# Performance work log

Hardware: AMD Instinct MI355X
Metric: run time of the kernel (lower is better)

The kernel has to match this reference:

```python
import jax, jax.numpy as jnp
import numpy as np

N_NODES = 100000
N_EDGES = 1600000
F_IN = 64
F_HID = 64
F_OUT = 64
N_HEADS = 4


def setup_inputs() -> dict:
    key = jax.random.key(0)
    ks = jax.random.split(key, 7)
    h = jax.random.normal(ks[0], (N_NODES, F_IN), dtype=jnp.float32)
    src = jax.random.randint(ks[1], (N_EDGES,), 0, N_NODES, dtype=jnp.int32)
    dst = jax.random.randint(ks[2], (N_EDGES,), 0, N_NODES, dtype=jnp.int32)
    s = 1.0 / np.sqrt(F_IN)
    Wk = jax.random.normal(ks[3], (F_IN, F_HID), dtype=jnp.float32) * s
    Wq = jax.random.normal(ks[4], (F_IN, F_HID), dtype=jnp.float32) * s
    W = jax.random.normal(ks[5], (F_IN, F_OUT), dtype=jnp.float32) * s
    b = jnp.zeros((F_OUT,), dtype=jnp.float32)
    return {"h": h, "src": src, "dst": dst, "Wk": Wk, "Wq": Wq, "W": W, "b": b,
            "num_heads": N_HEADS}


def reference(h, src, dst, Wk, Wq, W, b, num_heads):
    N = h.shape[0]
    H = num_heads
    # k, q: [N, H, Dh]
    k = (h @ Wk).reshape(N, H, -1)
    q = (h @ Wq).reshape(N, H, -1)
    # edge scores e[e,h] = <k[src], q[dst]>  (u_dot_v)
    e = jnp.einsum('ehd,ehd->eh', k[src], q[dst])  # [E, H]
    # edge softmax over incoming edges of each destination node (per head)
    m = jax.ops.segment_max(e, dst, num_segments=N)          # [N, H]
    m = jax.lax.stop_gradient(m)
    ex = jnp.exp(e - m[dst])                                  # [E, H]
    z = jax.ops.segment_sum(ex, dst, num_segments=N)          # [N, H]
    a = ex / z[dst]                                           # [E, H]
    # message m = u_mul_e(h, a): broadcast (F,) with (H,1) -> [E, H, F]; sum to dst
    msg = h[src][:, None, :] * a[:, :, None]                  # [E, H, F]
    hn = jax.ops.segment_sum(msg, dst, num_segments=N)        # [N, H, F]
    out = hn @ W + b                                          # [N, H, F_out]
    return out.reshape(N, -1)                                 # [N, H*F_out]
```

## Files before the change

### kernel.cpp

```cpp
#include <hip/hip_runtime.h>
#include <hip/hip_fp16.h>
#include <math.h>


#define FDIM 64
#define NHEADS 4
#define TILE 8192
#define BCAP 6144

typedef float f32x2 __attribute__((ext_vector_type(2)));

__global__ __launch_bounds__(256) void k1_kernel(
    const float* __restrict__ h, const float* __restrict__ Wk,
    const float* __restrict__ Wq, const float* __restrict__ Wo,
    const int* __restrict__ src, const int* __restrict__ dst,
    __half* __restrict__ k16, __half* __restrict__ q16,
    __half* __restrict__ hp16, int* __restrict__ gcnt,
    unsigned int* __restrict__ ebuf,
    int N, int E, int KQB, int PB, int nbuck)
{
    __shared__ __align__(16) unsigned char smem_raw[39936];
    int bid = blockIdx.x;
    int t = threadIdx.x;
    if (bid < KQB) {
        float* sWk = (float*)smem_raw;
        float* sWq = (float*)(smem_raw + 16384);
        for (int i = t; i < FDIM * FDIM; i += 256) {
            sWk[i] = Wk[i] * 1.4426950408889634f;
            sWq[i] = Wq[i];
        }
        __syncthreads();
        int cg = t & 3;
        int rg = t >> 2;
        long base = (long)bid * 128 + rg * 2;
        const float4* sWk4 = (const float4*)sWk;
        const float4* sWq4 = (const float4*)sWq;
        const float4* h4 = (const float4*)h;
        float acck[2][16], accq[2][16];
#pragma unroll
        for (int i = 0; i < 2; ++i)
#pragma unroll
            for (int c = 0; c < 16; ++c) { acck[i][c] = 0.f; accq[i][c] = 0.f; }

        for (int fs = 0; fs < FDIM; fs += 4) {
            float4 hv[2];
#pragma unroll
            for (int i = 0; i < 2; ++i) {
                long r = base + i; if (r >= N) r = N - 1;
                hv[i] = h4[r * 16 + (fs >> 2)];
            }
#pragma unroll
            for (int fi = 0; fi < 4; ++fi) {
                int f = fs + fi;
                float4 wk0 = sWk4[f * 16 + cg * 4 + 0];
                float4 wk1 = sWk4[f * 16 + cg * 4 + 1];
                float4 wk2 = sWk4[f * 16 + cg * 4 + 2];
                float4 wk3 = sWk4[f * 16 + cg * 4 + 3];
                float4 wq0 = sWq4[f * 16 + cg * 4 + 0];
                float4 wq1 = sWq4[f * 16 + cg * 4 + 1];
                float4 wq2 = sWq4[f * 16 + cg * 4 + 2];
                float4 wq3 = sWq4[f * 16 + cg * 4 + 3];
#pragma unroll
                for (int i = 0; i < 2; ++i) {
                    float hvf = (&hv[i].x)[fi];
                    acck[i][0]  = fmaf(hvf, wk0.x, acck[i][0]);
                    acck[i][1]  = fmaf(hvf, wk0.y, acck[i][1]);
                    acck[i][2]  = fmaf(hvf, wk0.z, acck[i][2]);
                    acck[i][3]  = fmaf(hvf, wk0.w, acck[i][3]);
                    acck[i][4]  = fmaf(hvf, wk1.x, acck[i][4]);
                    acck[i][5]  = fmaf(hvf, wk1.y, acck[i][5]);
                    acck[i][6]  = fmaf(hvf, wk1.z, acck[i][6]);
                    acck[i][7]  = fmaf(hvf, wk1.w, acck[i][7]);
                    acck[i][8]  = fmaf(hvf, wk2.x, acck[i][8]);
                    acck[i][9]  = fmaf(hvf, wk2.y, acck[i][9]);
                    acck[i][10] = fmaf(hvf, wk2.z, acck[i][10]);
                    acck[i][11] = fmaf(hvf, wk2.w, acck[i][11]);
                    acck[i][12] = fmaf(hvf, wk3.x, acck[i][12]);
                    acck[i][13] = fmaf(hvf, wk3.y, acck[i][13]);
                    acck[i][14] = fmaf(hvf, wk3.z, acck[i][14]);
                    acck[i][15] = fmaf(hvf, wk3.w, acck[i][15]);
                    accq[i][0]  = fmaf(hvf, wq0.x, accq[i][0]);
                    accq[i][1]  = fmaf(hvf, wq0.y, accq[i][1]);
                    accq[i][2]  = fmaf(hvf, wq0.z, accq[i][2]);
                    accq[i][3]  = fmaf(hvf, wq0.w, accq[i][3]);
                    accq[i][4]  = fmaf(hvf, wq1.x, accq[i][4]);
                    accq[i][5]  = fmaf(hvf, wq1.y, accq[i][5]);
                    accq[i][6]  = fmaf(hvf, wq1.z, accq[i][6]);
                    accq[i][7]  = fmaf(hvf, wq1.w, accq[i][7]);
                    accq[i][8]  = fmaf(hvf, wq2.x, accq[i][8]);
                    accq[i][9]  = fmaf(hvf, wq2.y, accq[i][9]);
                    accq[i][10] = fmaf(hvf, wq2.z, accq[i][10]);
                    accq[i][11] = fmaf(hvf, wq2.w, accq[i][11]);
                    accq[i][12] = fmaf(hvf, wq3.x, accq[i][12]);
                    accq[i][13] = fmaf(hvf, wq3.y, accq[i][13]);
                    accq[i][14] = fmaf(hvf, wq3.z, accq[i][14]);
                    accq[i][15] = fmaf(hvf, wq3.w, accq[i][15]);
                }
            }
        }
#pragma unroll
        for (int i = 0; i < 2; ++i) {
            long r = base + i;
            if (r >= N) continue;
            __half2 hk[8], hq[8];
#pragma unroll
            for (int c = 0; c < 8; ++c) {
                hk[c] = __floats2half2_rn(acck[i][2 * c], acck[i][2 * c + 1]);
                hq[c] = __floats2half2_rn(accq[i][2 * c], accq[i][2 * c + 1]);
            }
            float4* kout = (float4*)(k16 + (size_t)r * FDIM + cg * 16);
            float4* qout = (float4*)(q16 + (size_t)r * FDIM + cg * 16);
            kout[0] = ((float4*)hk)[0]; kout[1] = ((float4*)hk)[1];
            qout[0] = ((float4*)hq)[0]; qout[1] = ((float4*)hq)[1];
        }
    } else if (bid < KQB + PB) {
        float* sW = (float*)smem_raw;
        for (int i = t; i < FDIM * FDIM; i += 256) sW[i] = Wo[i];
        __syncthreads();
        int cg = t & 3;
        int rg = t >> 2;
        long base = (long)(bid - KQB) * 128 + rg * 2;
        const float4* sW4 = (const float4*)sW;
        const float4* h4 = (const float4*)h;
        float accp[2][16];
#pragma unroll
        for (int i = 0; i < 2; ++i)
#pragma unroll
            for (int c = 0; c < 16; ++c) accp[i][c] = 0.f;

        for (int fs = 0; fs < FDIM; fs += 4) {
            float4 hv[2];
#pragma unroll
            for (int i = 0; i < 2; ++i) {
                long r = base + i; if (r >= N) r = N - 1;
                hv[i] = h4[r * 16 + (fs >> 2)];
            }
#pragma unroll
            for (int fi = 0; fi < 4; ++fi) {
                int f = fs + fi;
                float4 w0 = sW4[f * 16 + cg * 4 + 0];
                float4 w1 = sW4[f * 16 + cg * 4 + 1];
                float4 w2 = sW4[f * 16 + cg * 4 + 2];
                float4 w3 = sW4[f * 16 + cg * 4 + 3];
#pragma unroll
                for (int i = 0; i < 2; ++i) {
                    float hvf = (&hv[i].x)[fi];
                    accp[i][0]  = fmaf(hvf, w0.x, accp[i][0]);
                    accp[i][1]  = fmaf(hvf, w0.y, accp[i][1]);
                    accp[i][2]  = fmaf(hvf, w0.z, accp[i][2]);
                    accp[i][3]  = fmaf(hvf, w0.w, accp[i][3]);
                    accp[i][4]  = fmaf(hvf, w1.x, accp[i][4]);
                    accp[i][5]  = fmaf(hvf, w1.y, accp[i][5]);
                    accp[i][6]  = fmaf(hvf, w1.z, accp[i][6]);
                    accp[i][7]  = fmaf(hvf, w1.w, accp[i][7]);
                    accp[i][8]  = fmaf(hvf, w2.x, accp[i][8]);
                    accp[i][9]  = fmaf(hvf, w2.y, accp[i][9]);
                    accp[i][10] = fmaf(hvf, w2.z, accp[i][10]);
                    accp[i][11] = fmaf(hvf, w2.w, accp[i][11]);
                    accp[i][12] = fmaf(hvf, w3.x, accp[i][12]);
                    accp[i][13] = fmaf(hvf, w3.y, accp[i][13]);
                    accp[i][14] = fmaf(hvf, w3.z, accp[i][14]);
                    accp[i][15] = fmaf(hvf, w3.w, accp[i][15]);
                }
            }
        }
#pragma unroll
        for (int i = 0; i < 2; ++i) {
            long r = base + i;
            if (r >= N) continue;
            __half2 hp[8];
#pragma unroll
            for (int c = 0; c < 8; ++c)
                hp[c] = __floats2half2_rn(accp[i][2 * c], accp[i][2 * c + 1]);
            float4* pout = (float4*)(hp16 + (size_t)r * FDIM + cg * 16);
            pout[0] = ((float4*)hp)[0];
            pout[1] = ((float4*)hp)[1];
        }
    } else {
        unsigned int* bh     = (unsigned int*)smem_raw;
        unsigned int* bstart = bh + 512;
        unsigned int* bbase  = bstart + 512;
        unsigned int* sd     = bbase + 512;
        unsigned int* ebuf_l = sd + 256;
        long e0 = (long)(bid - KQB - PB) * TILE;
        int cnt_tile = (int)(((long)E - e0 < (long)TILE) ? ((long)E - e0) : (long)TILE);

        bh[t] = 0; bh[t + 256] = 0;
        __syncthreads();
        for (int j = t; j < cnt_tile; j += 256)
            atomicAdd(&bh[dst[e0 + j] >> 8], 1u);
        __syncthreads();
        unsigned int c0 = bh[2 * t], c1 = bh[2 * t + 1];
        unsigned int s = c0 + c1;
        sd[t] = s;
        __syncthreads();
        for (int off = 1; off < 256; off <<= 1) {
            unsigned int v = (t >= off) ? sd[t - off] : 0;
            __syncthreads();
            sd[t] += v;
            __syncthreads();
        }
        unsigned int ex = sd[t] - s;
        bh[2 * t] = ex;          bstart[2 * t] = ex;
        bh[2 * t + 1] = ex + c0; bstart[2 * t + 1] = ex + c0;
        if (c0 > 0) bbase[2 * t] = (unsigned int)atomicAdd(&gcnt[2 * t], (int)c0);
        if (c1 > 0) bbase[2 * t + 1] = (unsigned int)atomicAdd(&gcnt[2 * t + 1], (int)c1);
        __syncthreads();
        for (int j = t; j < cnt_tile; j += 256) {
            int d = dst[e0 + j];
            int sv = src[e0 + j];
            unsigned int pos = atomicAdd(&bh[d >> 8], 1u);
            ebuf_l[pos] = ((unsigned int)sv << 8) | (unsigned int)(d & 255);
        }
        __syncthreads();
        int wave = t >> 6, lane = t & 63;
        for (int b = wave; b < nbuck; b += 4) {
            unsigned int st = bstart[b];
            unsigned int en = bh[b];
            if (st == en) continue;
            unsigned int gb = bbase[b];
            if (gb >= (unsigned int)BCAP) continue;
            unsigned int room = (unsigned int)BCAP - gb;
            if (en - st > room) en = st + room;
            unsigned int* dstp = ebuf + (size_t)b * BCAP + gb;
            for (unsigned int j = st + lane; j < en; j += 64)
                dstp[j - st] = ebuf_l[j];
        }
    }
}

__global__ __launch_bounds__(256) void binB_kernel(
    const int* __restrict__ gcnt, const unsigned int* __restrict__ ebuf,
    int* __restrict__ rowptr, int* __restrict__ srcs, int N)
{
    __shared__ int sg[512];
    __shared__ unsigned int lh[256];
    __shared__ unsigned int sd[256];
    __shared__ unsigned int srcs_l[BCAP];
    int t = threadIdx.x;
    int b = blockIdx.x;

    int c0 = gcnt[2 * t], c1 = gcnt[2 * t + 1];
    int ssum = c0 + c1;
    sd[t] = (unsigned int)ssum;
    __syncthreads();
    for (int off = 1; off < 256; off <<= 1) {
        unsigned int v = (t >= off) ? sd[t - off] : 0;
        __syncthreads();
        sd[t] += v;
        __syncthreads();
    }
    int ex = (int)sd[t] - ssum;
    sg[2 * t] = ex;
    sg[2 * t + 1] = ex + c0;
    __syncthreads();
    int gb = sg[b];
    int cnt = gcnt[b];
    if (cnt > BCAP) cnt = BCAP;
    int n0 = b << 8;
    const unsigned int* eb = ebuf + (size_t)b * BCAP;

    lh[t] = 0;
    __syncthreads();
    for (int j = t; j < cnt; j += 256)
        atomicAdd(&lh[eb[j] & 255u], 1u);
    __syncthreads();
    unsigned int c = lh[t];
    sd[t] = c;
    __syncthreads();
    for (int off = 1; off < 256; off <<= 1) {
        unsigned int v = (t >= off) ? sd[t - off] : 0;
        __syncthreads();
        sd[t] += v;
        __syncthreads();
    }
    unsigned int excl = sd[t] - c;
    lh[t] = excl;
    if (n0 + t < N) rowptr[n0 + t] = gb + (int)excl;
    __syncthreads();
    for (int j = t; j < cnt; j += 256) {
        unsigned int p = eb[j];
        unsigned int pos = atomicAdd(&lh[p & 255u], 1u);
        srcs_l[pos] = p >> 8;
    }
    __syncthreads();
    for (int j = t; j < cnt; j += 256)
        srcs[gb + j] = (int)srcs_l[j];
}

__device__ __forceinline__ float dot16(const float4* kk, const float* qf) {
    const __half2* kh = (const __half2*)kk;
    float acc = 0.f;
#pragma unroll
    for (int j = 0; j < 8; ++j) {
        float2 kf = __half22float2(kh[j]);
        acc = fmaf(kf.x, qf[2 * j], acc);
        acc = fmaf(kf.y, qf[2 * j + 1], acc);
    }
    return acc;
}

__device__ __forceinline__ void agg2f(
    float w0, float w1, float w2, float w3, __half2 g,
    f32x2& a0, f32x2& a1, f32x2& a2, f32x2& a3)
{
    float2 f2 = __half22float2(g);
    f32x2 hv; hv.x = f2.x; hv.y = f2.y;
    f32x2 wv;
    wv.x = w0; wv.y = w0; a0 = __builtin_elementwise_fma(wv, hv, a0);
    wv.x = w1; wv.y = w1; a1 = __builtin_elementwise_fma(wv, hv, a1);
    wv.x = w2; wv.y = w2; a2 = __builtin_elementwise_fma(wv, hv, a2);
    wv.x = w3; wv.y = w3; a3 = __builtin_elementwise_fma(wv, hv, a3);
}

__global__ __launch_bounds__(256) void fused_sa_kernel(
    const int* __restrict__ rowptr, const int* __restrict__ srcs,
    const __half* __restrict__ k16, const __half* __restrict__ q16,
    const __half* __restrict__ hp16, const float* __restrict__ bvec,
    float* __restrict__ out, int N, int E)
{
    int lane = threadIdx.x & 63;
    int n = blockIdx.x * 4 + (threadIdx.x >> 6);
    if (n >= N) return;
    int start = rowptr[n];
    int end   = (n == N - 1) ? E : rowptr[n + 1];

    int hh   = lane & 3;
    int rr   = lane >> 2;
    int half = lane >> 5;
    int fl   = lane & 31;

    const float4* qp = (const float4*)(q16 + (size_t)n * FDIM + hh * 16);
    float4 qv[2] = { qp[0], qp[1] };
    const __half2* qh = (const __half2*)qv;
    float qf[16];
#pragma unroll
    for (int j = 0; j < 8; ++j) {
        float2 f = __half22float2(qh[j]);
        qf[2 * j] = f.x;
        qf[2 * j + 1] = f.y;
    }

    float zacc = 0.f;
    f32x2 a0 = {0.f, 0.f}, a1 = {0.f, 0.f}, a2 = {0.f, 0.f}, a3 = {0.f, 0.f};

    for (int base = start; base < end; base += 16) {
        int idx = base + rr;
        bool valid = (idx < end);
        int ic = valid ? idx : (end - 1);
        int sA = srcs[ic];
        const float4* kp = (const float4*)(k16 + (size_t)sA * FDIM + hh * 16);
        float4 ka[2] = { kp[0], kp[1] };
        float w = __builtin_amdgcn_exp2f(dot16(ka, qf));
        w = valid ? w : 0.f;
        zacc += w;

#pragma unroll
        for (int j = 0; j < 2; ++j) {
            int g0i = base + j * 8;
            if (g0i < end) {
                int rb = j * 8 + half;
                int s0 = __shfl(sA, (rb + 0) * 4, 64);
                int s1 = __shfl(sA, (rb + 2) * 4, 64);
                int s2 = __shfl(sA, (rb + 4) * 4, 64);
                int s3 = __shfl(sA, (rb + 6) * 4, 64);
                __half2 g0 = *((const __half2*)(hp16 + (size_t)s0 * FDIM) + fl);
                __half2 g1 = *((const __half2*)(hp16 + (size_t)s1 * FDIM) + fl);
                __half2 g2 = *((const __half2*)(hp16 + (size_t)s2 * FDIM) + fl);
                __half2 g3 = *((const __half2*)(hp16 + (size_t)s3 * FDIM) + fl);
                float wa0 = __shfl(w, (rb + 0) * 4 + 0, 64);
                float wa1 = __shfl(w, (rb + 0) * 4 + 1, 64);
                float wa2 = __shfl(w, (rb + 0) * 4 + 2, 64);
                float wa3 = __shfl(w, (rb + 0) * 4 + 3, 64);
                agg2f(wa0, wa1, wa2, wa3, g0, a0, a1, a2, a3);
                float wb0 = __shfl(w, (rb + 2) * 4 + 0, 64);
                float wb1 = __shfl(w, (rb + 2) * 4 + 1, 64);
                float wb2 = __shfl(w, (rb + 2) * 4 + 2, 64);
                float wb3 = __shfl(w, (rb + 2) * 4 + 3, 64);
                agg2f(wb0, wb1, wb2, wb3, g1, a0, a1, a2, a3);
                float wc0 = __shfl(w, (rb + 4) * 4 + 0, 64);
                float wc1 = __shfl(w, (rb + 4) * 4 + 1, 64);
                float wc2 = __shfl(w, (rb + 4) * 4 + 2, 64);
                float wc3 = __shfl(w, (rb + 4) * 4 + 3, 64);
                agg2f(wc0, wc1, wc2, wc3, g2, a0, a1, a2, a3);
                float wd0 = __shfl(w, (rb + 6) * 4 + 0, 64);
                float wd1 = __shfl(w, (rb + 6) * 4 + 1, 64);
                float wd2 = __shfl(w, (rb + 6) * 4 + 2, 64);
                float wd3 = __shfl(w, (rb + 6) * 4 + 3, 64);
                agg2f(wd0, wd1, wd2, wd3, g3, a0, a1, a2, a3);
            }
        }
    }

    zacc += __shfl_xor(zacc, 4, 64);
    zacc += __shfl_xor(zacc, 8, 64);
    zacc += __shfl_xor(zacc, 16, 64);
    zacc += __shfl_xor(zacc, 32, 64);
    float z0 = __shfl(zacc, 0, 64);
    float z1 = __shfl(zacc, 1, 64);
    float z2 = __shfl(zacc, 2, 64);
    float z3 = __shfl(zacc, 3, 64);

    a0.x += __shfl_xor(a0.x, 32, 64); a0.y += __shfl_xor(a0.y, 32, 64);
    a1.x += __shfl_xor(a1.x, 32, 64); a1.y += __shfl_xor(a1.y, 32, 64);
    a2.x += __shfl_xor(a2.x, 32, 64); a2.y += __shfl_xor(a2.y, 32, 64);
    a3.x += __shfl_xor(a3.x, 32, 64); a3.y += __shfl_xor(a3.y, 32, 64);

    if (half != 0) return;
    float bv0 = bvec[2 * fl], bv1 = bvec[2 * fl + 1];
    float2* o = (float2*)(out + (size_t)n * (NHEADS * FDIM));
    if (end > start) {
        float rz0 = 1.f / z0;
        float rz1 = 1.f / z1;
        float rz2 = 1.f / z2;
        float rz3 = 1.f / z3;
        o[fl]      = make_float2(fmaf(a0.x, rz0, bv0), fmaf(a0.y, rz0, bv1));
        o[32 + fl] = make_float2(fmaf(a1.x, rz1, bv0), fmaf(a1.y, rz1, bv1));
        o[64 + fl] = make_float2(fmaf(a2.x, rz2, bv0), fmaf(a2.y, rz2, bv1));
        o[96 + fl] = make_float2(fmaf(a3.x, rz3, bv0), fmaf(a3.y, rz3, bv1));
    } else {
        float2 bz = make_float2(bv0, bv1);
        o[fl] = bz; o[32 + fl] = bz; o[64 + fl] = bz; o[96 + fl] = bz;
    }
}

extern "C" void kernel_launch(void* const* d_in, const int* in_sizes, int n_in,
                              void* d_out, int out_size, void* d_ws, size_t ws_size,
                              hipStream_t stream) {
    const float* h   = (const float*)d_in[0];
    const int*   src = (const int*)d_in[1];
    const int*   dst = (const int*)d_in[2];
    const float* Wk  = (const float*)d_in[3];
    const float* Wq  = (const float*)d_in[4];
    const float* W   = (const float*)d_in[5];
    const float* b   = (const float*)d_in[6];
    float* out = (float*)d_out;

    const int N = in_sizes[0] / FDIM;
    const int E = in_sizes[1];

    const int NBUCK = (N + 255) >> 8;
    const int NTILE = (E + TILE - 1) / TILE;
    const int KQB   = (N + 127) / 128;
    const int PB    = (N + 127) / 128;

    __half* k16 = (__half*)d_ws;
    __half* q16 = k16 + (size_t)N * FDIM;
    __half* hp16 = q16 + (size_t)N * FDIM;
    unsigned int* ebuf = (unsigned int*)(hp16 + (size_t)N * FDIM);
    int* srcs   = (int*)(ebuf + (size_t)NBUCK * BCAP);
    int* gcnt   = srcs + E;
    int* rowptr = gcnt + 512;

    hipMemsetAsync(gcnt, 0, 512 * sizeof(int), stream);

    k1_kernel<<<KQB + PB + NTILE, 256, 0, stream>>>(
        h, Wk, Wq, W, src, dst, k16, q16, hp16, gcnt, ebuf,
        N, E, KQB, PB, NBUCK);
    binB_kernel<<<NBUCK, 256, 0, stream>>>(gcnt, ebuf, rowptr, srcs, N);
    fused_sa_kernel<<<(N + 3) / 4, 256, 0, stream>>>(
        rowptr, srcs, k16, q16, hp16, b, out, N, E);
}
```

Baseline: 332.5 us.

## Use 8-byte gathers with four edges per wave step and cache bucket entries in LDS

The aggregation loop in the fused kernel now splits the wave into four quarter-waves, each gathering a 4-half (8-byte) slice of a source row. It processes one edge per quarter per step, giving four iterations of one load instead of two iterations of four 4-byte loads. That means fewer but wider gather instructions and fewer weight shuffles per edge, with twice the accumulators and a two-stage cross-lane reduction at the end. Separately, binB now keeps the bucket's edge list in shared memory after the first read so the scatter pass does not re-read global memory, at the cost of an extra 24KB of LDS per block.

New measurement: 317.4 us. -4.6%, faster.

```diff
diff --git a/kernel.cpp b/kernel.cpp
--- a/kernel.cpp
+++ b/kernel.cpp
@@ -236,6 +236,7 @@
     __shared__ int sg[512];
     __shared__ unsigned int lh[256];
     __shared__ unsigned int sd[256];
+    __shared__ unsigned int ebuf_l[BCAP];
     __shared__ unsigned int srcs_l[BCAP];
     int t = threadIdx.x;
     int b = blockIdx.x;
@@ -243,6 +244,7 @@
     int c0 = gcnt[2 * t], c1 = gcnt[2 * t + 1];
     int ssum = c0 + c1;
     sd[t] = (unsigned int)ssum;
+    lh[t] = 0;
     __syncthreads();
     for (int off = 1; off < 256; off <<= 1) {
         unsigned int v = (t >= off) ? sd[t - off] : 0;
@@ -260,10 +262,11 @@
     int n0 = b << 8;
     const unsigned int* eb = ebuf + (size_t)b * BCAP;
 
-    lh[t] = 0;
-    __syncthreads();
-    for (int j = t; j < cnt; j += 256)
-        atomicAdd(&lh[eb[j] & 255u], 1u);
+    for (int j = t; j < cnt; j += 256) {
+        unsigned int p = eb[j];
+        ebuf_l[j] = p;
+        atomicAdd(&lh[p & 255u], 1u);
+    }
     __syncthreads();
     unsigned int c = lh[t];
     sd[t] = c;
@@ -279,7 +282,7 @@
     if (n0 + t < N) rowptr[n0 + t] = gb + (int)excl;
     __syncthreads();
     for (int j = t; j < cnt; j += 256) {
-        unsigned int p = eb[j];
+        unsigned int p = ebuf_l[j];
         unsigned int pos = atomicAdd(&lh[p & 255u], 1u);
         srcs_l[pos] = p >> 8;
     }
@@ -298,19 +301,6 @@
         acc = fmaf(kf.y, qf[2 * j + 1], acc);
     }
     return acc;
-}
-
-__device__ __forceinline__ void agg2f(
-    float w0, float w1, float w2, float w3, __half2 g,
-    f32x2& a0, f32x2& a1, f32x2& a2, f32x2& a3)
-{
-    float2 f2 = __half22float2(g);
-    f32x2 hv; hv.x = f2.x; hv.y = f2.y;
-    f32x2 wv;
-    wv.x = w0; wv.y = w0; a0 = __builtin_elementwise_fma(wv, hv, a0);
-    wv.x = w1; wv.y = w1; a1 = __builtin_elementwise_fma(wv, hv, a1);
-    wv.x = w2; wv.y = w2; a2 = __builtin_elementwise_fma(wv, hv, a2);
-    wv.x = w3; wv.y = w3; a3 = __builtin_elementwise_fma(wv, hv, a3);
 }
 
 __global__ __launch_bounds__(256) void fused_sa_kernel(
@@ -325,10 +315,10 @@
     int start = rowptr[n];
     int end   = (n == N - 1) ? E : rowptr[n + 1];
 
-    int hh   = lane & 3;
-    int rr   = lane >> 2;
-    int half = lane >> 5;
-    int fl   = lane & 31;
+    int hh = lane & 3;
+    int rr = lane >> 2;
+    int qt = lane >> 4;
+    int fq = lane & 15;
 
     const float4* qp = (const float4*)(q16 + (size_t)n * FDIM + hh * 16);
     float4 qv[2] = { qp[0], qp[1] };
@@ -342,7 +332,10 @@
     }
 
     float zacc = 0.f;
-    f32x2 a0 = {0.f, 0.f}, a1 = {0.f, 0.f}, a2 = {0.f, 0.f}, a3 = {0.f, 0.f};
+    f32x2 a00 = {0.f,0.f}, a01 = {0.f,0.f};
+    f32x2 a10 = {0.f,0.f}, a11 = {0.f,0.f};
+    f32x2 a20 = {0.f,0.f}, a21 = {0.f,0.f};
+    f32x2 a30 = {0.f,0.f}, a31 = {0.f,0.f};
 
     for (int base = start; base < end; base += 16) {
         int idx = base + rr;
@@ -356,38 +349,32 @@
         zacc += w;
 
 #pragma unroll
-        for (int j = 0; j < 2; ++j) {
-            int g0i = base + j * 8;
-            if (g0i < end) {
-                int rb = j * 8 + half;
-                int s0 = __shfl(sA, (rb + 0) * 4, 64);
-                int s1 = __shfl(sA, (rb + 2) * 4, 64);
-                int s2 = __shfl(sA, (rb + 4) * 4, 64);
-                int s3 = __shfl(sA, (rb + 6) * 4, 64);
-                __half2 g0 = *((const __half2*)(hp16 + (size_t)s0 * FDIM) + fl);
-                __half2 g1 = *((const __half2*)(hp16 + (size_t)s1 * FDIM) + fl);
-                __half2 g2 = *((const __half2*)(hp16 + (size_t)s2 * FDIM) + fl);
-                __half2 g3 = *((const __half2*)(hp16 + (size_t)s3 * FDIM) + fl);
-                float wa0 = __shfl(w, (rb + 0) * 4 + 0, 64);
-                float wa1 = __shfl(w, (rb + 0) * 4 + 1, 64);
-                float wa2 = __shfl(w, (rb + 0) * 4 + 2, 64);
-                float wa3 = __shfl(w, (rb + 0) * 4 + 3, 64);
-                agg2f(wa0, wa1, wa2, wa3, g0, a0, a1, a2, a3);
-                float wb0 = __shfl(w, (rb + 2) * 4 + 0, 64);
-                float wb1 = __shfl(w, (rb + 2) * 4 + 1, 64);
-                float wb2 = __shfl(w, (rb + 2) * 4 + 2, 64);
-                float wb3 = __shfl(w, (rb + 2) * 4 + 3, 64);
-                agg2f(wb0, wb1, wb2, wb3, g1, a0, a1, a2, a3);
-                float wc0 = __shfl(w, (rb + 4) * 4 + 0, 64);
-                float wc1 = __shfl(w, (rb + 4) * 4 + 1, 64);
-                float wc2 = __shfl(w, (rb + 4) * 4 + 2, 64);
-                float wc3 = __shfl(w, (rb + 4) * 4 + 3, 64);
-                agg2f(wc0, wc1, wc2, wc3, g2, a0, a1, a2, a3);
-                float wd0 = __shfl(w, (rb + 6) * 4 + 0, 64);
-                float wd1 = __shfl(w, (rb + 6) * 4 + 1, 64);
-                float wd2 = __shfl(w, (rb + 6) * 4 + 2, 64);
-                float wd3 = __shfl(w, (rb + 6) * 4 + 3, 64);
-                agg2f(wd0, wd1, wd2, wd3, g3, a0, a1, a2, a3);
+        for (int k = 0; k < 4; ++k) {
+            if (base + k * 4 < end) {
+                int rloc = k * 4 + qt;
+                int sB = __shfl(sA, rloc * 4, 64);
+                uint2 g = *(const uint2*)(hp16 + (size_t)sB * FDIM + fq * 4);
+                float w0 = __shfl(w, rloc * 4 + 0, 64);
+                float w1 = __shfl(w, rloc * 4 + 1, 64);
+                float w2 = __shfl(w, rloc * 4 + 2, 64);
+                float w3 = __shfl(w, rloc * 4 + 3, 64);
+                float2 flo = __half22float2(*(__half2*)&g.x);
+                float2 fhi = __half22float2(*(__half2*)&g.y);
+                f32x2 vlo; vlo.x = flo.x; vlo.y = flo.y;
+                f32x2 vhi; vhi.x = fhi.x; vhi.y = fhi.y;
+                f32x2 wv;
+                wv.x = w0; wv.y = w0;
+                a00 = __builtin_elementwise_fma(wv, vlo, a00);
+                a01 = __builtin_elementwise_fma(wv, vhi, a01);
+                wv.x = w1; wv.y = w1;
+                a10 = __builtin_elementwise_fma(wv, vlo, a10);
+                a11 = __builtin_elementwise_fma(wv, vhi, a11);
+                wv.x = w2; wv.y = w2;
+                a20 = __builtin_elementwise_fma(wv, vlo, a20);
+                a21 = __builtin_elementwise_fma(wv, vhi, a21);
+                wv.x = w3; wv.y = w3;
+                a30 = __builtin_elementwise_fma(wv, vlo, a30);
+                a31 = __builtin_elementwise_fma(wv, vhi, a31);
             }
         }
     }
@@ -401,26 +388,30 @@
     float z2 = __shfl(zacc, 2, 64);
     float z3 = __shfl(zacc, 3, 64);
 
-    a0.x += __shfl_xor(a0.x, 32, 64); a0.y += __shfl_xor(a0.y, 32, 64);
-    a1.x += __shfl_xor(a1.x, 32, 64); a1.y += __shfl_xor(a1.y, 32, 64);
-    a2.x += __shfl_xor(a2.x, 32, 64); a2.y += __shfl_xor(a2.y, 32, 64);
-    a3.x += __shfl_xor(a3.x, 32, 64); a3.y += __shfl_xor(a3.y, 32, 64);
-
-    if (half != 0) return;
-    float bv0 = bvec[2 * fl], bv1 = bvec[2 * fl + 1];
-    float2* o = (float2*)(out + (size_t)n * (NHEADS * FDIM));
+#define MQ(A) \
+    (A).x += __shfl_xor((A).x, 16, 64); (A).y += __shfl_xor((A).y, 16, 64); \
+    (A).x += __shfl_xor((A).x, 32, 64); (A).y += __shfl_xor((A).y, 32, 64);
+    MQ(a00) MQ(a01) MQ(a10) MQ(a11) MQ(a20) MQ(a21) MQ(a30) MQ(a31)
+#undef MQ
+
+    if (qt != 0) return;
+    float4 bv = *(const float4*)(bvec + fq * 4);
+    float4* o = (float4*)(out + (size_t)n * (NHEADS * FDIM));
     if (end > start) {
         float rz0 = 1.f / z0;
         float rz1 = 1.f / z1;
         float rz2 = 1.f / z2;
         float rz3 = 1.f / z3;
-        o[fl]      = make_float2(fmaf(a0.x, rz0, bv0), fmaf(a0.y, rz0, bv1));
-        o[32 + fl] = make_float2(fmaf(a1.x, rz1, bv0), fmaf(a1.y, rz1, bv1));
-        o[64 + fl] = make_float2(fmaf(a2.x, rz2, bv0), fmaf(a2.y, rz2, bv1));
-        o[96 + fl] = make_float2(fmaf(a3.x, rz3, bv0), fmaf(a3.y, rz3, bv1));
+        o[fq] = make_float4(fmaf(a00.x, rz0, bv.x), fmaf(a00.y, rz0, bv.y),
+                            fmaf(a01.x, rz0, bv.z), fmaf(a01.y, rz0, bv.w));
+        o[16 + fq] = make_float4(fmaf(a10.x, rz1, bv.x), fmaf(a10.y, rz1, bv.y),
+                                 fmaf(a11.x, rz1, bv.z), fmaf(a11.y, rz1, bv.w));
+        o[32 + fq] = make_float4(fmaf(a20.x, rz2, bv.x), fmaf(a20.y, rz2, bv.y),
+                                 fmaf(a21.x, rz2, bv.z), fmaf(a21.y, rz2, bv.w));
+        o[48 + fq] = make_float4(fmaf(a30.x, rz3, bv.x), fmaf(a30.y, rz3, bv.y),
+                                 fmaf(a31.x, rz3, bv.z), fmaf(a31.y, rz3, bv.w));
     } else {
-        float2 bz = make_float2(bv0, bv1);
-        o[fl] = bz; o[32 + fl] = bz; o[64 + fl] = bz; o[96 + fl] = bz;
+        o[fq] = bv; o[16 + fq] = bv; o[32 + fq] = bv; o[48 + fq] = bv;
     }
 }
 
```
